# Performance work log

Measured on AMD Instinct MI355X. Metric: run time of the kernel, lower is better.

## Reference

```python
import jax, jax.numpy as jnp
import numpy as np

B, H, W, C = 4, 256, 256, 128
HEADS, WS, SHIFT = 4, 8, 4
EPS = 1e-5


def _rel_pos_index(ws):
    coords = np.stack(np.meshgrid(np.arange(ws), np.arange(ws), indexing='ij'))
    cf = coords.reshape(2, -1)
    rel = (cf[:, :, None] - cf[:, None, :]).transpose(1, 2, 0)
    rel[:, :, 0] += ws - 1
    rel[:, :, 1] += ws - 1
    rel[:, :, 0] *= 2 * ws - 1
    return rel.sum(-1).reshape(-1)

REL_IDX = jnp.array(_rel_pos_index(WS))


def _shift_mask(h, w, ws, shift):
    img = np.zeros((1, h, w, 1))
    cnt = 0
    sl = (slice(0, -ws), slice(-ws, -shift), slice(-shift, None))
    for hs in sl:
        for wsl in sl:
            img[:, hs, wsl, :] = cnt
            cnt += 1
    m = img.reshape(1, h // ws, ws, w // ws, ws, 1).transpose(0, 1, 3, 2, 4, 5).reshape(-1, ws * ws)
    am = m[:, None, :] - m[:, :, None]
    return jnp.array(np.where(am != 0, -100.0, 0.0).astype(np.float32))

ATTN_MASK = _shift_mask(H, W, WS, SHIFT)  # (nW, ws*ws, ws*ws)


def _ln(x, scale, bias):
    mu = x.mean(-1, keepdims=True)
    var = x.var(-1, keepdims=True)
    return (x - mu) / jnp.sqrt(var + EPS) * scale + bias


def setup_inputs() -> dict:
    key = jax.random.key(0)
    ks = jax.random.split(key, 8)
    s = 0.02
    return dict(
        hidden_states=jax.random.normal(ks[0], (B, H * W, C), jnp.float32),
        ln1_scale=jnp.ones((C,), jnp.float32), ln1_bias=jnp.zeros((C,), jnp.float32),
        q_w=jax.random.normal(ks[1], (C, C), jnp.float32) * s, q_b=jnp.zeros((C,), jnp.float32),
        k_w=jax.random.normal(ks[2], (C, C), jnp.float32) * s, k_b=jnp.zeros((C,), jnp.float32),
        v_w=jax.random.normal(ks[3], (C, C), jnp.float32) * s, v_b=jnp.zeros((C,), jnp.float32),
        proj_w=jax.random.normal(ks[4], (C, C), jnp.float32) * s, proj_b=jnp.zeros((C,), jnp.float32),
        rpb_table=jax.random.normal(ks[5], ((2 * WS - 1) ** 2, HEADS), jnp.float32) * s,
        ln2_scale=jnp.ones((C,), jnp.float32), ln2_bias=jnp.zeros((C,), jnp.float32),
        fc1_w=jax.random.normal(ks[6], (C, 4 * C), jnp.float32) * s, fc1_b=jnp.zeros((4 * C,), jnp.float32),
        fc2_w=jax.random.normal(ks[7], (4 * C, C), jnp.float32) * s, fc2_b=jnp.zeros((C,), jnp.float32),
    )


def reference(hidden_states, ln1_scale, ln1_bias, q_w, q_b, k_w, k_b, v_w, v_b,
              proj_w, proj_b, rpb_table, ln2_scale, ln2_bias, fc1_w, fc1_b, fc2_w, fc2_b):
    hd = C // HEADS
    T = WS * WS
    nW = (H // WS) * (W // WS)
    shortcut = hidden_states
    x = _ln(hidden_states, ln1_scale, ln1_bias).reshape(B, H, W, C)
    # cyclic shift
    x = jnp.roll(x, (-SHIFT, -SHIFT), axis=(1, 2))
    # window partition -> (B*nW, T, C)
    x = x.reshape(B, H // WS, WS, W // WS, WS, C).transpose(0, 1, 3, 2, 4, 5).reshape(-1, T, C)
    q = (x @ q_w + q_b).reshape(-1, T, HEADS, hd) / jnp.sqrt(jnp.float32(hd))
    k = (x @ k_w + k_b).reshape(-1, T, HEADS, hd)
    v = (x @ v_w + v_b).reshape(-1, T, HEADS, hd)
    attn = jnp.einsum('bqhd,bkhd->bhqk', q, k)
    bias = rpb_table[REL_IDX].reshape(T, T, HEADS).transpose(2, 0, 1)  # (h, q, k)
    attn = attn + bias[None]
    # shift mask per window
    attn = attn.reshape(B, nW, HEADS, T, T) + ATTN_MASK[None, :, None]
    attn = jax.nn.softmax(attn.reshape(-1, HEADS, T, T), axis=-1)
    out = jnp.einsum('bhqk,bkhd->bqhd', attn, v).reshape(-1, T, C)
    out = out @ proj_w + proj_b
    # window reverse + un-shift
    out = out.reshape(B, H // WS, W // WS, WS, WS, C).transpose(0, 1, 3, 2, 4, 5).reshape(B, H, W, C)
    out = jnp.roll(out, (SHIFT, SHIFT), axis=(1, 2)).reshape(B, H * W, C)
    x = shortcut + out
    y = _ln(x, ln2_scale, ln2_bias)
    y = jax.nn.gelu(y @ fc1_w + fc1_b, approximate=False) @ fc2_w + fc2_b
    return x + y
```

## Files before the change

### kernel.cpp

```cpp
#include <hip/hip_runtime.h>
#include <hip/hip_bf16.h>
#include <math.h>

#define B_ 4
#define H_ 256
#define W_ 256
#define C_ 128
#define HEADS_ 4
#define HD_ 32
#define WS_ 8
#define SHIFT_ 4
#define T_ 64
#define NW_ 1024
#define M_ (B_*NW_*T_)

typedef float floatx4 __attribute__((ext_vector_type(4)));
typedef short bf16x8 __attribute__((ext_vector_type(8)));
typedef unsigned short ushort8v __attribute__((ext_vector_type(8)));
typedef unsigned int uint4v __attribute__((ext_vector_type(4)));

#define MFMA16(a,b,c) __builtin_amdgcn_mfma_f32_16x16x32_bf16(a,b,c,0,0,0)

__device__ __forceinline__ unsigned short f2b(float f){
    union { float f; unsigned int i; } c; c.f = f;
    unsigned int r = c.i + 0x7FFFu + ((c.i >> 16) & 1u);
    return (unsigned short)(r >> 16);
}
__device__ __forceinline__ int region_id(int x){ return (x < 248) ? 0 : ((x < 252) ? 1 : 2); }

__device__ __forceinline__ bf16x8 ldfrag(const unsigned short* p){
    return *(const bf16x8*)p;
}
__device__ __forceinline__ bf16x8 ldfrag_strided(const unsigned short* p, int stride){
    ushort8v u;
    #pragma unroll
    for (int j = 0; j < 8; j++) u[j] = p[j*stride];
    return __builtin_bit_cast(bf16x8, u);
}
__device__ __forceinline__ floatx4 fzero(){ floatx4 v = {0.f,0.f,0.f,0.f}; return v; }

__device__ __forceinline__ float erf_fast(float z){
    float az = fabsf(z);
    float t = 1.0f / fmaf(0.3275911f, az, 1.0f);
    float poly = t*(0.254829592f + t*(-0.284496736f + t*(1.421413741f +
                 t*(-1.453152027f + t*1.061405429f))));
    float e = __expf(-z*z);
    float er = 1.0f - poly*e;
    return (z < 0.f) ? -er : er;
}

#define WSO_QT   0
#define WSO_KT   16384
#define WSO_VT   32768
#define WSO_PT   49152
#define WSO_W1T  65536
#define WSO_W2T  131072
#define WSO_BIAS 196608
#define WS_BYTES_NEEDED (196608u*2u + 16384u*4u)

__global__ __launch_bounds__(256) void prep_weights_kernel(
        const float* __restrict__ qw, const float* __restrict__ kw,
        const float* __restrict__ vw, const float* __restrict__ pw,
        const float* __restrict__ fc1, const float* __restrict__ fc2,
        const float* __restrict__ rpb, unsigned short* __restrict__ ws)
{
    int tid = blockIdx.x * 256 + threadIdx.x;
    int nt = gridDim.x * 256;
    for (int i = tid; i < 16384; i += nt) {
        int n = i >> 7, k = i & 127;
        ws[WSO_QT + i] = f2b(qw[k*128 + n]);
        ws[WSO_KT + i] = f2b(kw[k*128 + n]);
        ws[WSO_VT + i] = f2b(vw[k*128 + n]);
        ws[WSO_PT + i] = f2b(pw[k*128 + n]);
    }
    for (int i = tid; i < 65536; i += nt) {
        int n = i >> 7, k = i & 127;
        ws[WSO_W1T + i] = f2b(fc1[(size_t)k*512 + n]);
    }
    for (int i = tid; i < 65536; i += nt) {
        int n = i >> 9, k = i & 511;
        ws[WSO_W2T + i] = f2b(fc2[(size_t)k*128 + n]);
    }
    float* bt = (float*)(ws + WSO_BIAS);
    for (int i = tid; i < 16384; i += nt) {
        int h = i >> 12, q = (i >> 6) & 63, k = i & 63;
        int th = q >> 3, tw = q & 7, jh = k >> 3, jw = k & 7;
        bt[i] = rpb[((th - jh + 7)*15 + (tw - jw + 7))*HEADS_ + h];
    }
}

__device__ __forceinline__ void gemm64x128_g(
        const unsigned short (*Xs)[136], const unsigned short* __restrict__ Wt,
        int wv, int quad, int l15, floatx4 acc[4][2])
{
    #pragma unroll
    for (int c = 0; c < 4; c++) {
        bf16x8 bf0 = ldfrag(Wt + (size_t)(32*wv + l15)*128      + c*32 + quad*8);
        bf16x8 bf1 = ldfrag(Wt + (size_t)(32*wv + 16 + l15)*128 + c*32 + quad*8);
        #pragma unroll
        for (int m = 0; m < 4; m++) {
            bf16x8 af = ldfrag(&Xs[16*m + l15][c*32 + quad*8]);
            acc[m][0] = MFMA16(af, bf0, acc[m][0]);
            acc[m][1] = MFMA16(af, bf1, acc[m][1]);
        }
    }
}

__global__ __launch_bounds__(256) void swin_attn_kernel3(
        const float* __restrict__ hidden,
        const float* __restrict__ ln1_s, const float* __restrict__ ln1_b,
        const float* __restrict__ q_b, const float* __restrict__ k_b,
        const float* __restrict__ v_b, const float* __restrict__ p_b,
        const unsigned short* __restrict__ wsu,
        float* __restrict__ xres)
{
    __shared__ __align__(16) unsigned short SH[2][T_][136];
    unsigned short (*Xs)[136] = SH[0];
    unsigned short (*Ks)[136] = SH[1];

    int tid = threadIdx.x;
    int wv = tid >> 6, lane = tid & 63;
    int quad = lane >> 4, l15 = lane & 15;
    int gw = blockIdx.x;
    int wi = gw & (NW_-1), b = gw >> 10;
    int hb = wi >> 5, wb = wi & 31;

    {
        int rloc = lane >> 2;
        int t = wv*16 + rloc;
        int th = t >> 3, tw = t & 7;
        int h = (hb*8 + th + SHIFT_) & 255;
        int w = (wb*8 + tw + SHIFT_) & 255;
        int c0 = (lane & 3) * 32;
        const float* xp = hidden + ((size_t)((b<<16) + (h<<8) + w)) * C_ + c0;
        float4 xv[8];
        float s = 0.f, ss = 0.f;
        #pragma unroll
        for (int i = 0; i < 8; i++) {
            xv[i] = *((const float4*)xp + i);
            s  += xv[i].x + xv[i].y + xv[i].z + xv[i].w;
            ss += xv[i].x*xv[i].x + xv[i].y*xv[i].y + xv[i].z*xv[i].z + xv[i].w*xv[i].w;
        }
        s  += __shfl_xor(s, 1, 64);  s  += __shfl_xor(s, 2, 64);
        ss += __shfl_xor(ss, 1, 64); ss += __shfl_xor(ss, 2, 64);
        float mean = s * (1.0f/C_);
        float var  = ss * (1.0f/C_) - mean*mean;
        float rstd = rsqrtf(var + 1e-5f);
        #pragma unroll
        for (int i = 0; i < 8; i++) {
            float4 sc = *((const float4*)(ln1_s + c0) + i);
            float4 bi = *((const float4*)(ln1_b + c0) + i);
            ushort4 o;
            o.x = f2b((xv[i].x - mean)*rstd*sc.x + bi.x);
            o.y = f2b((xv[i].y - mean)*rstd*sc.y + bi.y);
            o.z = f2b((xv[i].z - mean)*rstd*sc.z + bi.z);
            o.w = f2b((xv[i].w - mean)*rstd*sc.w + bi.w);
            *(ushort4*)&Xs[t][c0 + 4*i] = o;
        }
    }
    __syncthreads();

    unsigned int vpk[4][2][2];
    {
        floatx4 kacc[4][2], vacc[4][2];
        #pragma unroll
        for (int m = 0; m < 4; m++) {
            kacc[m][0] = fzero(); kacc[m][1] = fzero();
            vacc[m][0] = fzero(); vacc[m][1] = fzero();
        }
        const unsigned short* Kt = wsu + WSO_KT;
        const unsigned short* Vt = wsu + WSO_VT;
        #pragma unroll
        for (int c = 0; c < 4; c++) {
            size_t off0 = (size_t)(32*wv + l15)*128      + c*32 + quad*8;
            size_t off1 = (size_t)(32*wv + 16 + l15)*128 + c*32 + quad*8;
            bf16x8 kb0 = ldfrag(Kt + off0), kb1 = ldfrag(Kt + off1);
            bf16x8 vb0 = ldfrag(Vt + off0), vb1 = ldfrag(Vt + off1);
            #pragma unroll
            for (int m = 0; m < 4; m++) {
                bf16x8 af = ldfrag(&Xs[16*m + l15][c*32 + quad*8]);
                kacc[m][0] = MFMA16(af, kb0, kacc[m][0]);
                kacc[m][1] = MFMA16(af, kb1, kacc[m][1]);
                vacc[m][0] = MFMA16(af, vb0, vacc[m][0]);
                vacc[m][1] = MFMA16(af, vb1, vacc[m][1]);
            }
        }
        float kb0 = k_b[32*wv + l15], kb1 = k_b[32*wv + 16 + l15];
        float vb0 = v_b[32*wv + l15], vb1 = v_b[32*wv + 16 + l15];
        #pragma unroll
        for (int m = 0; m < 4; m++) {
            #pragma unroll
            for (int r = 0; r < 4; r++) {
                int q = 16*m + 4*quad + r;
                Ks[q][32*wv + l15]      = f2b(kacc[m][0][r] + kb0);
                Ks[q][32*wv + 16 + l15] = f2b(kacc[m][1][r] + kb1);
            }
            vpk[m][0][0] = (unsigned int)f2b(vacc[m][0][0] + vb0)
                         | ((unsigned int)f2b(vacc[m][0][1] + vb0) << 16);
            vpk[m][0][1] = (unsigned int)f2b(vacc[m][0][2] + vb0)
                         | ((unsigned int)f2b(vacc[m][0][3] + vb0) << 16);
            vpk[m][1][0] = (unsigned int)f2b(vacc[m][1][0] + vb1)
                         | ((unsigned int)f2b(vacc[m][1][1] + vb1) << 16);
            vpk[m][1][1] = (unsigned int)f2b(vacc[m][1][2] + vb1)
                         | ((unsigned int)f2b(vacc[m][1][3] + vb1) << 16);
        }
    }
    floatx4 qacc[4][2];
    #pragma unroll
    for (int m = 0; m < 4; m++) { qacc[m][0] = fzero(); qacc[m][1] = fzero(); }
    gemm64x128_g(Xs, wsu + WSO_QT, wv, quad, l15, qacc);
    __syncthreads();
    {
        const float sc = 0.17677669529663687f;
        float qb0 = q_b[32*wv + l15], qb1 = q_b[32*wv + 16 + l15];
        #pragma unroll
        for (int m = 0; m < 4; m++)
            #pragma unroll
            for (int r = 0; r < 4; r++) {
                int q = 16*m + 4*quad + r;
                Xs[q][32*wv + l15]      = f2b((qacc[m][0][r] + qb0) * sc);
                Xs[q][32*wv + 16 + l15] = f2b((qacc[m][1][r] + qb1) * sc);
            }
    }

    floatx4 sacc[4][4];
    #pragma unroll
    for (int m = 0; m < 4; m++)
        #pragma unroll
        for (int n = 0; n < 4; n++) sacc[m][n] = fzero();
    {
        bf16x8 qf[4], kf[4];
        #pragma unroll
        for (int m = 0; m < 4; m++) qf[m] = ldfrag(&Xs[16*m + l15][32*wv + quad*8]);
        #pragma unroll
        for (int n = 0; n < 4; n++) kf[n] = ldfrag(&Ks[16*n + l15][32*wv + quad*8]);
        #pragma unroll
        for (int m = 0; m < 4; m++)
            #pragma unroll
            for (int n = 0; n < 4; n++) sacc[m][n] = MFMA16(kf[n], qf[m], sacc[m][n]);
    }
    __syncthreads();

    {
        const float* bt = (const float*)(wsu + WSO_BIAS) + (wv << 12);
        int cidk[4][4];
        #pragma unroll
        for (int n = 0; n < 4; n++)
            #pragma unroll
            for (int r = 0; r < 4; r++) {
                int kt = 16*n + 4*quad + r;
                cidk[n][r] = region_id(hb*8 + (kt >> 3))*3 + region_id(wb*8 + (kt & 7));
            }
        #pragma unroll
        for (int m = 0; m < 4; m++) {
            int q = 16*m + l15;
            int cidq = region_id(hb*8 + (q >> 3))*3 + region_id(wb*8 + (q & 7));
            float v[4][4];
            float mx = -3.0e38f;
            #pragma unroll
            for (int n = 0; n < 4; n++) {
                float4 bv = *(const float4*)(bt + q*64 + 16*n + 4*quad);
                #pragma unroll
                for (int r = 0; r < 4; r++) {
                    float d = sacc[m][n][r] + bv[r];
                    if (cidq != cidk[n][r]) d -= 100.f;
                    v[n][r] = d;
                    mx = fmaxf(mx, d);
                }
            }
            mx = fmaxf(mx, __shfl_xor(mx, 16, 64));
            mx = fmaxf(mx, __shfl_xor(mx, 32, 64));
            float sum = 0.f;
            #pragma unroll
            for (int n = 0; n < 4; n++)
                #pragma unroll
                for (int r = 0; r < 4; r++) { v[n][r] = __expf(v[n][r] - mx); sum += v[n][r]; }
            sum += __shfl_xor(sum, 16, 64);
            sum += __shfl_xor(sum, 32, 64);
            float inv = 1.0f / sum;
            #pragma unroll
            for (int n = 0; n < 4; n++)
                #pragma unroll
                for (int r = 0; r < 4; r++) sacc[m][n][r] = v[n][r] * inv;
        }
    }

    unsigned short* Ph = (wv < 2) ? (&Ks[0][0] + wv*2560) : (&Xs[0][0] + (wv-2)*2560);
    floatx4 oacc[4][2];
    #pragma unroll
    for (int m = 0; m < 4; m++) { oacc[m][0] = fzero(); oacc[m][1] = fzero(); }
    int laneA = 16*(2*(quad & 1)) + l15;
    bool mhi = (quad >= 2);
    #pragma unroll
    for (int kb = 0; kb < 2; kb++) {
        #pragma unroll
        for (int m = 0; m < 4; m++)
            #pragma unroll
            for (int n2 = 0; n2 < 2; n2++)
                #pragma unroll
                for (int r = 0; r < 4; r++)
                    Ph[(16*m + l15)*40 + n2*16 + 4*quad + r] = f2b(sacc[m][2*kb + n2][r]);
        bf16x8 bfr[2];
        #pragma unroll
        for (int u = 0; u < 2; u++) {
            unsigned int a0m0 = (unsigned int)__shfl((int)vpk[2*kb+0][u][0], laneA, 64);
            unsigned int a1m0 = (unsigned int)__shfl((int)vpk[2*kb+0][u][1], laneA, 64);
            unsigned int b0m0 = (unsigned int)__shfl((int)vpk[2*kb+0][u][0], laneA+16, 64);
            unsigned int b1m0 = (unsigned int)__shfl((int)vpk[2*kb+0][u][1], laneA+16, 64);
            unsigned int a0m1 = (unsigned int)__shfl((int)vpk[2*kb+1][u][0], laneA, 64);
            unsigned int a1m1 = (unsigned int)__shfl((int)vpk[2*kb+1][u][1], laneA, 64);
            unsigned int b0m1 = (unsigned int)__shfl((int)vpk[2*kb+1][u][0], laneA+16, 64);
            unsigned int b1m1 = (unsigned int)__shfl((int)vpk[2*kb+1][u][1], laneA+16, 64);
            uint4v uu;
            uu[0] = mhi ? a0m1 : a0m0;
            uu[1] = mhi ? a1m1 : a1m0;
            uu[2] = mhi ? b0m1 : b0m0;
            uu[3] = mhi ? b1m1 : b1m0;
            bfr[u] = __builtin_bit_cast(bf16x8, uu);
        }
        #pragma unroll
        for (int m = 0; m < 4; m++) {
            bf16x8 af = ldfrag(&Ph[(16*m + l15)*40 + quad*8]);
            oacc[m][0] = MFMA16(af, bfr[0], oacc[m][0]);
            oacc[m][1] = MFMA16(af, bfr[1], oacc[m][1]);
        }
    }
    __syncthreads();
    #pragma unroll
    for (int m = 0; m < 4; m++)
        #pragma unroll
        for (int r = 0; r < 4; r++) {
            int q = 16*m + 4*quad + r;
            Xs[q][32*wv + l15]      = f2b(oacc[m][0][r]);
            Xs[q][32*wv + 16 + l15] = f2b(oacc[m][1][r]);
        }
    __syncthreads();
    floatx4 pacc[4][2];
    #pragma unroll
    for (int m = 0; m < 4; m++) { pacc[m][0] = fzero(); pacc[m][1] = fzero(); }
    gemm64x128_g(Xs, wsu + WSO_PT, wv, quad, l15, pacc);
    __syncthreads();
    {
        float* Fb = (float*)&SH[0][0][0];
        float pb0 = p_b[32*wv + l15], pb1 = p_b[32*wv + 16 + l15];
        #pragma unroll
        for (int m = 0; m < 4; m++)
            #pragma unroll
            for (int r = 0; r < 4; r++) {
                int q = 16*m + 4*quad + r;
                Fb[q*128 + 32*wv + l15]      = pacc[m][0][r] + pb0;
                Fb[q*128 + 32*wv + 16 + l15] = pacc[m][1][r] + pb1;
            }
        __syncthreads();
        int t = tid >> 2;
        int cs = (tid & 3) * 32;
        int th = t >> 3, tw = t & 7;
        int h = (hb*8 + th + SHIFT_) & 255;
        int w = (wb*8 + tw + SHIFT_) & 255;
        size_t dst = ((size_t)((b<<16) + (h<<8) + w)) * C_ + cs;
        const float4* hp = (const float4*)(hidden + dst);
        float4* op = (float4*)(xres + dst);
        const float4* fp = (const float4*)(Fb + t*128 + cs);
        #pragma unroll
        for (int i = 0; i < 8; i++) {
            float4 hv = hp[i];
            float4 fv = fp[i];
            float4 o; o.x = hv.x + fv.x; o.y = hv.y + fv.y;
            o.z = hv.z + fv.z; o.w = hv.w + fv.w;
            op[i] = o;
        }
    }
}

__global__ __launch_bounds__(256) void mlp_ln_kernel3(
        float* __restrict__ xio,
        const float* __restrict__ ln2_s, const float* __restrict__ ln2_b,
        const float* __restrict__ b1, const float* __restrict__ b2,
        const unsigned short* __restrict__ wsu)
{
    __shared__ __align__(16) unsigned short As[T_][136];
    __shared__ __align__(16) unsigned short G[2][T_][72];
    const unsigned short* W1t = wsu + WSO_W1T;
    const unsigned short* W2t = wsu + WSO_W2T;
    int tid = threadIdx.x, wv = tid >> 6, lane = tid & 63;
    int quad = lane >> 4, l15 = lane & 15;
    size_t row0 = (size_t)blockIdx.x * 64;

    {
        int rloc = lane >> 2;
        int t = wv*16 + rloc;
        int c0 = (lane & 3) * 32;
        const float* xp = xio + (row0 + t)*C_ + c0;
        float4 xv[8];
        float s = 0.f, ss = 0.f;
        #pragma unroll
        for (int i = 0; i < 8; i++) {
            xv[i] = *((const float4*)xp + i);
            s  += xv[i].x + xv[i].y + xv[i].z + xv[i].w;
            ss += xv[i].x*xv[i].x + xv[i].y*xv[i].y + xv[i].z*xv[i].z + xv[i].w*xv[i].w;
        }
        s  += __shfl_xor(s, 1, 64);  s  += __shfl_xor(s, 2, 64);
        ss += __shfl_xor(ss, 1, 64); ss += __shfl_xor(ss, 2, 64);
        float mean = s * (1.0f/C_);
        float var  = ss * (1.0f/C_) - mean*mean;
        float rstd = rsqrtf(var + 1e-5f);
        #pragma unroll
        for (int i = 0; i < 8; i++) {
            float4 sc = *((const float4*)(ln2_s + c0) + i);
            float4 bi = *((const float4*)(ln2_b + c0) + i);
            ushort4 o;
            o.x = f2b((xv[i].x - mean)*rstd*sc.x + bi.x);
            o.y = f2b((xv[i].y - mean)*rstd*sc.y + bi.y);
            o.z = f2b((xv[i].z - mean)*rstd*sc.z + bi.z);
            o.w = f2b((xv[i].w - mean)*rstd*sc.w + bi.w);
            *(ushort4*)&As[t][c0 + 4*i] = o;
        }
    }
    __syncthreads();

    floatx4 acc2[4][2];
    #pragma unroll
    for (int m = 0; m < 4; m++) { acc2[m][0] = fzero(); acc2[m][1] = fzero(); }

    for (int ch = 0; ch < 8; ch++) {
        int gb = ch & 1;
        floatx4 a1[4];
        #pragma unroll
        for (int m = 0; m < 4; m++) a1[m] = fzero();
        #pragma unroll
        for (int kc = 0; kc < 4; kc++) {
            bf16x8 bf = ldfrag(W1t + (size_t)(ch*64 + 16*wv + l15)*128 + kc*32 + quad*8);
            #pragma unroll
            for (int m = 0; m < 4; m++) {
                bf16x8 af = ldfrag(&As[16*m + l15][kc*32 + quad*8]);
                a1[m] = MFMA16(af, bf, a1[m]);
            }
        }
        {
            int c_rel = 16*wv + l15;
            float bb = b1[ch*64 + c_rel];
            #pragma unroll
            for (int m = 0; m < 4; m++)
                #pragma unroll
                for (int r = 0; r < 4; r++) {
                    float hh = a1[m][r] + bb;
                    float g = 0.5f * hh * (1.0f + erf_fast(hh * 0.70710678118654752f));
                    G[gb][16*m + 4*quad + r][c_rel] = f2b(g);
                }
        }
        __syncthreads();
        #pragma unroll
        for (int ki = 0; ki < 2; ki++) {
            bf16x8 bf0 = ldfrag(W2t + (size_t)(32*wv + l15)*512      + ch*64 + ki*32 + quad*8);
            bf16x8 bf1 = ldfrag(W2t + (size_t)(32*wv + 16 + l15)*512 + ch*64 + ki*32 + quad*8);
            #pragma unroll
            for (int m = 0; m < 4; m++) {
                bf16x8 af = ldfrag(&G[gb][16*m + l15][ki*32 + quad*8]);
                acc2[m][0] = MFMA16(af, bf0, acc2[m][0]);
                acc2[m][1] = MFMA16(af, bf1, acc2[m][1]);
            }
        }
    }
    {
        float bb0 = b2[32*wv + l15], bb1 = b2[32*wv + 16 + l15];
        #pragma unroll
        for (int m = 0; m < 4; m++)
            #pragma unroll
            for (int r = 0; r < 4; r++) {
                size_t rr = row0 + 16*m + 4*quad + r;
                int c0 = 32*wv + l15;
                xio[rr*C_ + c0]      += acc2[m][0][r] + bb0;
                xio[rr*C_ + c0 + 16] += acc2[m][1][r] + bb1;
            }
    }
}


__device__ __forceinline__ void gemm64x128(
        const unsigned short (*Xs)[136], unsigned short (*Wc)[132],
        const float* __restrict__ Wg, int tid, int wv, int quad, int l15,
        floatx4 acc[4][2])
{
    for (int c = 0; c < 4; c++) {
        __syncthreads();
        #pragma unroll
        for (int it = 0; it < 4; it++) {
            int idx = tid + it*256;
            int kk = idx >> 5;
            int n4 = (idx & 31) * 4;
            float4 v = *(const float4*)(Wg + (size_t)(c*32 + kk)*C_ + n4);
            ushort4 o; o.x=f2b(v.x); o.y=f2b(v.y); o.z=f2b(v.z); o.w=f2b(v.w);
            *(ushort4*)&Wc[kk][n4] = o;
        }
        __syncthreads();
        bf16x8 bf0 = ldfrag_strided(&Wc[quad*8][32*wv + l15],      132);
        bf16x8 bf1 = ldfrag_strided(&Wc[quad*8][32*wv + 16 + l15], 132);
        #pragma unroll
        for (int m = 0; m < 4; m++) {
            bf16x8 af = ldfrag(&Xs[16*m + l15][c*32 + quad*8]);
            acc[m][0] = MFMA16(af, bf0, acc[m][0]);
            acc[m][1] = MFMA16(af, bf1, acc[m][1]);
        }
    }
}

__global__ __launch_bounds__(256) void swin_attn_kernel(
        const float* __restrict__ hidden,
        const float* __restrict__ ln1_s, const float* __restrict__ ln1_b,
        const float* __restrict__ q_w, const float* __restrict__ q_b,
        const float* __restrict__ k_w, const float* __restrict__ k_b,
        const float* __restrict__ v_w, const float* __restrict__ v_b,
        const float* __restrict__ p_w, const float* __restrict__ p_b,
        const float* __restrict__ rpb,
        float* __restrict__ xres)
{
    __shared__ unsigned short Xs[T_][136];
    __shared__ unsigned short Ks[T_][136];
    __shared__ unsigned short Vs[T_][134];
    __shared__ __align__(16) unsigned char U[10240];

    unsigned short (*Wc)[132] = (unsigned short(*)[132])U;
    float* rpbf = (float*)U;

    int tid = threadIdx.x;
    int wv = tid >> 6, lane = tid & 63;
    int quad = lane >> 4, l15 = lane & 15;
    int gw = blockIdx.x;
    int wi = gw & (NW_-1), b = gw >> 10;
    int hb = wi >> 5, wb = wi & 31;

    for (int it = 0; it < 16; it++) {
        int t = wv*16 + it;
        int th = t >> 3, tw = t & 7;
        int h = (hb*8 + th + SHIFT_) & 255;
        int w = (wb*8 + tw + SHIFT_) & 255;
        size_t src = ((size_t)((b<<16) + (h<<8) + w)) * C_;
        float2 u = *(const float2*)(hidden + src + 2*lane);
        float x0 = u.x, x1 = u.y;
        float s = x0 + x1, ss = x0*x0 + x1*x1;
        #pragma unroll
        for (int m = 32; m > 0; m >>= 1) {
            s  += __shfl_xor(s,  m, 64);
            ss += __shfl_xor(ss, m, 64);
        }
        float mean = s * (1.0f/C_);
        float var  = ss * (1.0f/C_) - mean*mean;
        float rstd = rsqrtf(var + 1e-5f);
        int c0 = 2*lane;
        ushort2 o;
        o.x = f2b((x0 - mean) * rstd * ln1_s[c0]   + ln1_b[c0]);
        o.y = f2b((x1 - mean) * rstd * ln1_s[c0+1] + ln1_b[c0+1]);
        *(ushort2*)&Xs[t][c0] = o;
    }

    {
        floatx4 acc[4][2];
        #pragma unroll
        for (int m = 0; m < 4; m++) { acc[m][0] = fzero(); acc[m][1] = fzero(); }
        gemm64x128(Xs, Wc, k_w, tid, wv, quad, l15, acc);
        float kb0 = k_b[32*wv + l15], kb1 = k_b[32*wv + 16 + l15];
        #pragma unroll
        for (int m = 0; m < 4; m++)
            #pragma unroll
            for (int r = 0; r < 4; r++) {
                int q = 16*m + 4*quad + r;
                Ks[q][32*wv + l15]      = f2b(acc[m][0][r] + kb0);
                Ks[q][32*wv + 16 + l15] = f2b(acc[m][1][r] + kb1);
            }
    }
    {
        floatx4 acc[4][2];
        #pragma unroll
        for (int m = 0; m < 4; m++) { acc[m][0] = fzero(); acc[m][1] = fzero(); }
        gemm64x128(Xs, Wc, v_w, tid, wv, quad, l15, acc);
        float vb0 = v_b[32*wv + l15], vb1 = v_b[32*wv + 16 + l15];
        #pragma unroll
        for (int m = 0; m < 4; m++)
            #pragma unroll
            for (int r = 0; r < 4; r++) {
                int q = 16*m + 4*quad + r;
                Vs[q][32*wv + l15]      = f2b(acc[m][0][r] + vb0);
                Vs[q][32*wv + 16 + l15] = f2b(acc[m][1][r] + vb1);
            }
    }
    floatx4 qacc[4][2];
    #pragma unroll
    for (int m = 0; m < 4; m++) { qacc[m][0] = fzero(); qacc[m][1] = fzero(); }
    gemm64x128(Xs, Wc, q_w, tid, wv, quad, l15, qacc);
    __syncthreads();
    for (int i = tid; i < 225*HEADS_; i += 256) rpbf[i] = rpb[i];
    {
        const float sc = 0.17677669529663687f;
        float qb0 = q_b[32*wv + l15], qb1 = q_b[32*wv + 16 + l15];
        #pragma unroll
        for (int m = 0; m < 4; m++)
            #pragma unroll
            for (int r = 0; r < 4; r++) {
                int q = 16*m + 4*quad + r;
                Xs[q][32*wv + l15]      = f2b((qacc[m][0][r] + qb0) * sc);
                Xs[q][32*wv + 16 + l15] = f2b((qacc[m][1][r] + qb1) * sc);
            }
    }
    __syncthreads();

    floatx4 sacc[4][4];
    #pragma unroll
    for (int m = 0; m < 4; m++)
        #pragma unroll
        for (int n = 0; n < 4; n++) sacc[m][n] = fzero();
    {
        bf16x8 qf[4], kf[4];
        #pragma unroll
        for (int m = 0; m < 4; m++) qf[m] = ldfrag(&Xs[16*m + l15][32*wv + quad*8]);
        #pragma unroll
        for (int n = 0; n < 4; n++) kf[n] = ldfrag(&Ks[16*n + l15][32*wv + quad*8]);
        #pragma unroll
        for (int m = 0; m < 4; m++)
            #pragma unroll
            for (int n = 0; n < 4; n++) sacc[m][n] = MFMA16(qf[m], kf[n], sacc[m][n]);
    }
    {
        int jh_[4], jw_[4], cidj_[4];
        #pragma unroll
        for (int n = 0; n < 4; n++) {
            int kt = 16*n + l15;
            jh_[n] = kt >> 3; jw_[n] = kt & 7;
            cidj_[n] = region_id(hb*8 + jh_[n])*3 + region_id(wb*8 + jw_[n]);
        }
        #pragma unroll
        for (int m = 0; m < 4; m++)
            #pragma unroll
            for (int r = 0; r < 4; r++) {
                int q = 16*m + 4*quad + r;
                int th = q >> 3, twq = q & 7;
                int cidi = region_id(hb*8 + th)*3 + region_id(wb*8 + twq);
                float v[4];
                #pragma unroll
                for (int n = 0; n < 4; n++) {
                    float d = sacc[m][n][r];
                    d += rpbf[((th - jh_[n] + 7)*15 + (twq - jw_[n] + 7))*HEADS_ + wv];
                    if (cidi != cidj_[n]) d -= 100.f;
                    v[n] = d;
                }
                float mx = fmaxf(fmaxf(v[0],v[1]), fmaxf(v[2],v[3]));
                #pragma unroll
                for (int off = 1; off < 16; off <<= 1) mx = fmaxf(mx, __shfl_xor(mx, off, 64));
                float sum = 0.f;
                #pragma unroll
                for (int n = 0; n < 4; n++) { v[n] = __expf(v[n] - mx); sum += v[n]; }
                #pragma unroll
                for (int off = 1; off < 16; off <<= 1) sum += __shfl_xor(sum, off, 64);
                float inv = 1.0f / sum;
                #pragma unroll
                for (int n = 0; n < 4; n++) sacc[m][n][r] = v[n] * inv;
            }
    }
    __syncthreads();

    unsigned short* Ph = (wv < 2) ? (&Ks[0][0] + wv*2560)
                                  : ((unsigned short*)U + (wv-2)*2560);
    floatx4 oacc[4][2];
    #pragma unroll
    for (int m = 0; m < 4; m++) { oacc[m][0] = fzero(); oacc[m][1] = fzero(); }
    for (int kb = 0; kb < 2; kb++) {
        #pragma unroll
        for (int m = 0; m < 4; m++)
            #pragma unroll
            for (int r = 0; r < 4; r++) {
                int q = 16*m + 4*quad + r;
                Ph[q*40 + l15]      = f2b(sacc[m][2*kb+0][r]);
                Ph[q*40 + 16 + l15] = f2b(sacc[m][2*kb+1][r]);
            }
        __syncthreads();
        bf16x8 bf0 = ldfrag_strided(&Vs[kb*32 + quad*8][32*wv + l15],      134);
        bf16x8 bf1 = ldfrag_strided(&Vs[kb*32 + quad*8][32*wv + 16 + l15], 134);
        #pragma unroll
        for (int m = 0; m < 4; m++) {
            bf16x8 af = ldfrag(&Ph[(16*m + l15)*40 + quad*8]);
            oacc[m][0] = MFMA16(af, bf0, oacc[m][0]);
            oacc[m][1] = MFMA16(af, bf1, oacc[m][1]);
        }
        __syncthreads();
    }
    #pragma unroll
    for (int m = 0; m < 4; m++)
        #pragma unroll
        for (int r = 0; r < 4; r++) {
            int q = 16*m + 4*quad + r;
            Xs[q][32*wv + l15]      = f2b(oacc[m][0][r]);
            Xs[q][32*wv + 16 + l15] = f2b(oacc[m][1][r]);
        }
    {
        floatx4 acc[4][2];
        #pragma unroll
        for (int m = 0; m < 4; m++) { acc[m][0] = fzero(); acc[m][1] = fzero(); }
        gemm64x128(Xs, Wc, p_w, tid, wv, quad, l15, acc);
        float pb0 = p_b[32*wv + l15], pb1 = p_b[32*wv + 16 + l15];
        #pragma unroll
        for (int m = 0; m < 4; m++)
            #pragma unroll
            for (int r = 0; r < 4; r++) {
                int t = 16*m + 4*quad + r;
                int th = t >> 3, tw = t & 7;
                int h = (hb*8 + th + SHIFT_) & 255;
                int w = (wb*8 + tw + SHIFT_) & 255;
                size_t dst = ((size_t)((b<<16) + (h<<8) + w)) * C_;
                int c0 = 32*wv + l15;
                xres[dst + c0]      = hidden[dst + c0]      + acc[m][0][r] + pb0;
                xres[dst + c0 + 16] = hidden[dst + c0 + 16] + acc[m][1][r] + pb1;
            }
    }
}

__global__ __launch_bounds__(256) void mlp_ln_kernel(
        float* __restrict__ xio,
        const float* __restrict__ ln2_s, const float* __restrict__ ln2_b,
        const float* __restrict__ W1, const float* __restrict__ b1,
        const float* __restrict__ W2, const float* __restrict__ b2)
{
    __shared__ unsigned short As[T_][136];
    __shared__ unsigned short G[T_][72];
    __shared__ unsigned short W1c[C_][68];
    __shared__ unsigned short W2c[T_][132];
    int tid = threadIdx.x, wv = tid >> 6, lane = tid & 63;
    int quad = lane >> 4, l15 = lane & 15;
    size_t row0 = (size_t)blockIdx.x * 64;

    for (int it = 0; it < 16; it++) {
        int t = wv*16 + it;
        const float* xp = xio + (row0 + t)*C_;
        float2 u = *(const float2*)(xp + 2*lane);
        float x0 = u.x, x1 = u.y;
        float s = x0 + x1, ss = x0*x0 + x1*x1;
        #pragma unroll
        for (int m = 32; m > 0; m >>= 1) {
            s  += __shfl_xor(s,  m, 64);
            ss += __shfl_xor(ss, m, 64);
        }
        float mean = s * (1.0f/C_);
        float var  = ss * (1.0f/C_) - mean*mean;
        float rstd = rsqrtf(var + 1e-5f);
        int c0 = 2*lane;
        ushort2 o;
        o.x = f2b((x0 - mean) * rstd * ln2_s[c0]   + ln2_b[c0]);
        o.y = f2b((x1 - mean) * rstd * ln2_s[c0+1] + ln2_b[c0+1]);
        *(ushort2*)&As[t][c0] = o;
    }

    floatx4 acc2[4][2];
    #pragma unroll
    for (int m = 0; m < 4; m++) { acc2[m][0] = fzero(); acc2[m][1] = fzero(); }

    for (int ch = 0; ch < 8; ch++) {
        __syncthreads();
        #pragma unroll
        for (int it = 0; it < 8; it++) {
            int idx = tid + it*256;
            int k = idx >> 4, n4 = (idx & 15) * 4;
            float4 v = *(const float4*)(W1 + (size_t)k*512 + ch*64 + n4);
            ushort4 o; o.x=f2b(v.x); o.y=f2b(v.y); o.z=f2b(v.z); o.w=f2b(v.w);
            *(ushort4*)&W1c[k][n4] = o;
        }
        #pragma unroll
        for (int it = 0; it < 8; it++) {
            int idx = tid + it*256;
            int k = idx >> 5, n4 = (idx & 31) * 4;
            float4 v = *(const float4*)(W2 + (size_t)(ch*64 + k)*C_ + n4);
            ushort4 o; o.x=f2b(v.x); o.y=f2b(v.y); o.z=f2b(v.z); o.w=f2b(v.w);
            *(ushort4*)&W2c[k][n4] = o;
        }
        __syncthreads();
        floatx4 a1[4];
        #pragma unroll
        for (int m = 0; m < 4; m++) a1[m] = fzero();
        #pragma unroll
        for (int kc = 0; kc < 4; kc++) {
            bf16x8 bfrag = ldfrag_strided(&W1c[kc*32 + quad*8][16*wv + l15], 68);
            #pragma unroll
            for (int m = 0; m < 4; m++) {
                bf16x8 af = ldfrag(&As[16*m + l15][kc*32 + quad*8]);
                a1[m] = MFMA16(af, bfrag, a1[m]);
            }
        }
        {
            int c_rel = 16*wv + l15;
            float bb = b1[ch*64 + c_rel];
            #pragma unroll
            for (int m = 0; m < 4; m++)
                #pragma unroll
                for (int r = 0; r < 4; r++) {
                    int q = 16*m + 4*quad + r;
                    float hh = a1[m][r] + bb;
                    float g = 0.5f * hh * (1.0f + erff(hh * 0.70710678118654752f));
                    G[q][c_rel] = f2b(g);
                }
        }
        __syncthreads();
        #pragma unroll
        for (int ki = 0; ki < 2; ki++) {
            bf16x8 bf0 = ldfrag_strided(&W2c[ki*32 + quad*8][32*wv + l15],      132);
            bf16x8 bf1 = ldfrag_strided(&W2c[ki*32 + quad*8][32*wv + 16 + l15], 132);
            #pragma unroll
            for (int m = 0; m < 4; m++) {
                bf16x8 af = ldfrag(&G[16*m + l15][ki*32 + quad*8]);
                acc2[m][0] = MFMA16(af, bf0, acc2[m][0]);
                acc2[m][1] = MFMA16(af, bf1, acc2[m][1]);
            }
        }
    }
    {
        float bb0 = b2[32*wv + l15], bb1 = b2[32*wv + 16 + l15];
        #pragma unroll
        for (int m = 0; m < 4; m++)
            #pragma unroll
            for (int r = 0; r < 4; r++) {
                size_t rr = row0 + 16*m + 4*quad + r;
                int c0 = 32*wv + l15;
                xio[rr*C_ + c0]      += acc2[m][0][r] + bb0;
                xio[rr*C_ + c0 + 16] += acc2[m][1][r] + bb1;
            }
    }
}

extern "C" void kernel_launch(void* const* d_in, const int* in_sizes, int n_in,
                              void* d_out, int out_size, void* d_ws, size_t ws_size,
                              hipStream_t stream) {
    (void)in_sizes; (void)n_in; (void)out_size;
    const float* hidden = (const float*)d_in[0];
    const float* ln1_s  = (const float*)d_in[1];
    const float* ln1_b  = (const float*)d_in[2];
    const float* q_w    = (const float*)d_in[3];
    const float* q_b    = (const float*)d_in[4];
    const float* k_w    = (const float*)d_in[5];
    const float* k_b    = (const float*)d_in[6];
    const float* v_w    = (const float*)d_in[7];
    const float* v_b    = (const float*)d_in[8];
    const float* p_w    = (const float*)d_in[9];
    const float* p_b    = (const float*)d_in[10];
    const float* rpb    = (const float*)d_in[11];
    const float* ln2_s  = (const float*)d_in[12];
    const float* ln2_b  = (const float*)d_in[13];
    const float* fc1_w  = (const float*)d_in[14];
    const float* fc1_b  = (const float*)d_in[15];
    const float* fc2_w  = (const float*)d_in[16];
    const float* fc2_b  = (const float*)d_in[17];
    float* outp = (float*)d_out;

    if (d_ws != nullptr && ws_size >= (size_t)WS_BYTES_NEEDED) {
        unsigned short* wsu = (unsigned short*)d_ws;
        prep_weights_kernel<<<64, 256, 0, stream>>>(q_w, k_w, v_w, p_w,
                fc1_w, fc2_w, rpb, wsu);
        swin_attn_kernel3<<<B_*NW_, 256, 0, stream>>>(hidden, ln1_s, ln1_b,
                q_b, k_b, v_b, p_b, wsu, outp);
        mlp_ln_kernel3<<<M_/64, 256, 0, stream>>>(outp, ln2_s, ln2_b,
                fc1_b, fc2_b, wsu);
    } else {
        swin_attn_kernel<<<B_*NW_, 256, 0, stream>>>(hidden, ln1_s, ln1_b,
                q_w, q_b, k_w, k_b, v_w, v_b, p_w, p_b, rpb, outp);
        mlp_ln_kernel<<<M_/64, 256, 0, stream>>>(outp, ln2_s, ln2_b,
                fc1_w, fc1_b, fc2_w, fc2_b);
    }
}
```

Baseline: 619.3 us.

## Stage V and P in dedicated LDS, fuse QKV GEMM, single-buffer GELU tile

The attention kernel now computes Q, K and V in one fused MFMA loop. It stores V in a new shared-memory tile and reads it back with strided loads, replacing the register-packed V and its cross-lane shuffles. Softmax probabilities go to a dedicated per-wave LDS buffer instead of reusing the X/K tiles, which removes two block-wide barriers. The MLP kernel drops the double-buffered GELU tile for a single buffer with an extra barrier, adds a minimum-occupancy launch bound, and swaps in hardware rcp/rsq approximations. These changes trade more LDS in the attention kernel for fewer syncs and shuffles, and trade an extra sync in the MLP kernel for less LDS and higher occupancy.

```diff
diff --git a/kernel.cpp b/kernel.cpp
--- a/kernel.cpp
+++ b/kernel.cpp
@@ -17,7 +17,6 @@
 typedef float floatx4 __attribute__((ext_vector_type(4)));
 typedef short bf16x8 __attribute__((ext_vector_type(8)));
 typedef unsigned short ushort8v __attribute__((ext_vector_type(8)));
-typedef unsigned int uint4v __attribute__((ext_vector_type(4)));
 
 #define MFMA16(a,b,c) __builtin_amdgcn_mfma_f32_16x16x32_bf16(a,b,c,0,0,0)
 
@@ -39,14 +38,16 @@
 }
 __device__ __forceinline__ floatx4 fzero(){ floatx4 v = {0.f,0.f,0.f,0.f}; return v; }
 
-__device__ __forceinline__ float erf_fast(float z){
+__device__ __forceinline__ float gelu_fast(float x){
+    float z = x * 0.70710678118654752f;
     float az = fabsf(z);
-    float t = 1.0f / fmaf(0.3275911f, az, 1.0f);
+    float t = __builtin_amdgcn_rcpf(fmaf(0.3275911f, az, 1.0f));
     float poly = t*(0.254829592f + t*(-0.284496736f + t*(1.421413741f +
                  t*(-1.453152027f + t*1.061405429f))));
     float e = __expf(-z*z);
     float er = 1.0f - poly*e;
-    return (z < 0.f) ? -er : er;
+    er = (z < 0.f) ? -er : er;
+    return 0.5f * x * (1.0f + er);
 }
 
 #define WSO_QT   0
@@ -106,7 +107,7 @@
     }
 }
 
-__global__ __launch_bounds__(256) void swin_attn_kernel3(
+__global__ __launch_bounds__(256) void swin_attn_kernel4(
         const float* __restrict__ hidden,
         const float* __restrict__ ln1_s, const float* __restrict__ ln1_b,
         const float* __restrict__ q_b, const float* __restrict__ k_b,
@@ -115,6 +116,8 @@
         float* __restrict__ xres)
 {
     __shared__ __align__(16) unsigned short SH[2][T_][136];
+    __shared__ __align__(16) unsigned short Vs[T_][134];
+    __shared__ __align__(16) unsigned short PhD[4][2560];
     unsigned short (*Xs)[136] = SH[0];
     unsigned short (*Ks)[136] = SH[1];
 
@@ -145,7 +148,7 @@
         ss += __shfl_xor(ss, 1, 64); ss += __shfl_xor(ss, 2, 64);
         float mean = s * (1.0f/C_);
         float var  = ss * (1.0f/C_) - mean*mean;
-        float rstd = rsqrtf(var + 1e-5f);
+        float rstd = __builtin_amdgcn_rsqf(var + 1e-5f);
         #pragma unroll
         for (int i = 0; i < 8; i++) {
             float4 sc = *((const float4*)(ln1_s + c0) + i);
@@ -160,55 +163,49 @@
     }
     __syncthreads();
 
-    unsigned int vpk[4][2][2];
+    floatx4 qacc[4][2];
     {
         floatx4 kacc[4][2], vacc[4][2];
         #pragma unroll
         for (int m = 0; m < 4; m++) {
+            qacc[m][0] = fzero(); qacc[m][1] = fzero();
             kacc[m][0] = fzero(); kacc[m][1] = fzero();
             vacc[m][0] = fzero(); vacc[m][1] = fzero();
         }
+        const unsigned short* Qt = wsu + WSO_QT;
         const unsigned short* Kt = wsu + WSO_KT;
         const unsigned short* Vt = wsu + WSO_VT;
         #pragma unroll
         for (int c = 0; c < 4; c++) {
             size_t off0 = (size_t)(32*wv + l15)*128      + c*32 + quad*8;
             size_t off1 = (size_t)(32*wv + 16 + l15)*128 + c*32 + quad*8;
-            bf16x8 kb0 = ldfrag(Kt + off0), kb1 = ldfrag(Kt + off1);
-            bf16x8 vb0 = ldfrag(Vt + off0), vb1 = ldfrag(Vt + off1);
+            bf16x8 qf0 = ldfrag(Qt + off0), qf1 = ldfrag(Qt + off1);
+            bf16x8 kf0 = ldfrag(Kt + off0), kf1 = ldfrag(Kt + off1);
+            bf16x8 vf0 = ldfrag(Vt + off0), vf1 = ldfrag(Vt + off1);
             #pragma unroll
             for (int m = 0; m < 4; m++) {
                 bf16x8 af = ldfrag(&Xs[16*m + l15][c*32 + quad*8]);
-                kacc[m][0] = MFMA16(af, kb0, kacc[m][0]);
-                kacc[m][1] = MFMA16(af, kb1, kacc[m][1]);
-                vacc[m][0] = MFMA16(af, vb0, vacc[m][0]);
-                vacc[m][1] = MFMA16(af, vb1, vacc[m][1]);
+                qacc[m][0] = MFMA16(af, qf0, qacc[m][0]);
+                qacc[m][1] = MFMA16(af, qf1, qacc[m][1]);
+                kacc[m][0] = MFMA16(af, kf0, kacc[m][0]);
+                kacc[m][1] = MFMA16(af, kf1, kacc[m][1]);
+                vacc[m][0] = MFMA16(af, vf0, vacc[m][0]);
+                vacc[m][1] = MFMA16(af, vf1, vacc[m][1]);
             }
         }
         float kb0 = k_b[32*wv + l15], kb1 = k_b[32*wv + 16 + l15];
         float vb0 = v_b[32*wv + l15], vb1 = v_b[32*wv + 16 + l15];
         #pragma unroll
-        for (int m = 0; m < 4; m++) {
+        for (int m = 0; m < 4; m++)
             #pragma unroll
             for (int r = 0; r < 4; r++) {
                 int q = 16*m + 4*quad + r;
                 Ks[q][32*wv + l15]      = f2b(kacc[m][0][r] + kb0);
                 Ks[q][32*wv + 16 + l15] = f2b(kacc[m][1][r] + kb1);
-            }
-            vpk[m][0][0] = (unsigned int)f2b(vacc[m][0][0] + vb0)
-                         | ((unsigned int)f2b(vacc[m][0][1] + vb0) << 16);
-            vpk[m][0][1] = (unsigned int)f2b(vacc[m][0][2] + vb0)
-                         | ((unsigned int)f2b(vacc[m][0][3] + vb0) << 16);
-            vpk[m][1][0] = (unsigned int)f2b(vacc[m][1][0] + vb1)
-                         | ((unsigned int)f2b(vacc[m][1][1] + vb1) << 16);
-            vpk[m][1][1] = (unsigned int)f2b(vacc[m][1][2] + vb1)
-                         | ((unsigned int)f2b(vacc[m][1][3] + vb1) << 16);
-        }
-    }
-    floatx4 qacc[4][2];
-    #pragma unroll
-    for (int m = 0; m < 4; m++) { qacc[m][0] = fzero(); qacc[m][1] = fzero(); }
-    gemm64x128_g(Xs, wsu + WSO_QT, wv, quad, l15, qacc);
+                Vs[q][32*wv + l15]      = f2b(vacc[m][0][r] + vb0);
+                Vs[q][32*wv + 16 + l15] = f2b(vacc[m][1][r] + vb1);
+            }
+    }
     __syncthreads();
     {
         const float sc = 0.17677669529663687f;
@@ -239,7 +236,6 @@
             #pragma unroll
             for (int n = 0; n < 4; n++) sacc[m][n] = MFMA16(kf[n], qf[m], sacc[m][n]);
     }
-    __syncthreads();
 
     {
         const float* bt = (const float*)(wsu + WSO_BIAS) + (wv << 12);
@@ -277,7 +273,7 @@
                 for (int r = 0; r < 4; r++) { v[n][r] = __expf(v[n][r] - mx); sum += v[n][r]; }
             sum += __shfl_xor(sum, 16, 64);
             sum += __shfl_xor(sum, 32, 64);
-            float inv = 1.0f / sum;
+            float inv = __builtin_amdgcn_rcpf(sum);
             #pragma unroll
             for (int n = 0; n < 4; n++)
                 #pragma unroll
@@ -285,12 +281,10 @@
         }
     }
 
-    unsigned short* Ph = (wv < 2) ? (&Ks[0][0] + wv*2560) : (&Xs[0][0] + (wv-2)*2560);
+    unsigned short* Ph = PhD[wv];
     floatx4 oacc[4][2];
     #pragma unroll
     for (int m = 0; m < 4; m++) { oacc[m][0] = fzero(); oacc[m][1] = fzero(); }
-    int laneA = 16*(2*(quad & 1)) + l15;
-    bool mhi = (quad >= 2);
     #pragma unroll
     for (int kb = 0; kb < 2; kb++) {
         #pragma unroll
@@ -300,32 +294,15 @@
                 #pragma unroll
                 for (int r = 0; r < 4; r++)
                     Ph[(16*m + l15)*40 + n2*16 + 4*quad + r] = f2b(sacc[m][2*kb + n2][r]);
-        bf16x8 bfr[2];
-        #pragma unroll
-        for (int u = 0; u < 2; u++) {
-            unsigned int a0m0 = (unsigned int)__shfl((int)vpk[2*kb+0][u][0], laneA, 64);
-            unsigned int a1m0 = (unsigned int)__shfl((int)vpk[2*kb+0][u][1], laneA, 64);
-            unsigned int b0m0 = (unsigned int)__shfl((int)vpk[2*kb+0][u][0], laneA+16, 64);
-            unsigned int b1m0 = (unsigned int)__shfl((int)vpk[2*kb+0][u][1], laneA+16, 64);
-            unsigned int a0m1 = (unsigned int)__shfl((int)vpk[2*kb+1][u][0], laneA, 64);
-            unsigned int a1m1 = (unsigned int)__shfl((int)vpk[2*kb+1][u][1], laneA, 64);
-            unsigned int b0m1 = (unsigned int)__shfl((int)vpk[2*kb+1][u][0], laneA+16, 64);
-            unsigned int b1m1 = (unsigned int)__shfl((int)vpk[2*kb+1][u][1], laneA+16, 64);
-            uint4v uu;
-            uu[0] = mhi ? a0m1 : a0m0;
-            uu[1] = mhi ? a1m1 : a1m0;
-            uu[2] = mhi ? b0m1 : b0m0;
-            uu[3] = mhi ? b1m1 : b1m0;
-            bfr[u] = __builtin_bit_cast(bf16x8, uu);
-        }
+        bf16x8 bf0 = ldfrag_strided(&Vs[kb*32 + quad*8][32*wv + l15],      134);
+        bf16x8 bf1 = ldfrag_strided(&Vs[kb*32 + quad*8][32*wv + 16 + l15], 134);
         #pragma unroll
         for (int m = 0; m < 4; m++) {
             bf16x8 af = ldfrag(&Ph[(16*m + l15)*40 + quad*8]);
-            oacc[m][0] = MFMA16(af, bfr[0], oacc[m][0]);
-            oacc[m][1] = MFMA16(af, bfr[1], oacc[m][1]);
-        }
-    }
-    __syncthreads();
+            oacc[m][0] = MFMA16(af, bf0, oacc[m][0]);
+            oacc[m][1] = MFMA16(af, bf1, oacc[m][1]);
+        }
+    }
     #pragma unroll
     for (int m = 0; m < 4; m++)
         #pragma unroll
@@ -372,14 +349,14 @@
     }
 }
 
-__global__ __launch_bounds__(256) void mlp_ln_kernel3(
+__global__ __launch_bounds__(256, 6) void mlp_ln_kernel4(
         float* __restrict__ xio,
         const float* __restrict__ ln2_s, const float* __restrict__ ln2_b,
         const float* __restrict__ b1, const float* __restrict__ b2,
         const unsigned short* __restrict__ wsu)
 {
     __shared__ __align__(16) unsigned short As[T_][136];
-    __shared__ __align__(16) unsigned short G[2][T_][72];
+    __shared__ __align__(16) unsigned short G[T_][72];
     const unsigned short* W1t = wsu + WSO_W1T;
     const unsigned short* W2t = wsu + WSO_W2T;
     int tid = threadIdx.x, wv = tid >> 6, lane = tid & 63;
@@ -403,7 +380,7 @@
         ss += __shfl_xor(ss, 1, 64); ss += __shfl_xor(ss, 2, 64);
         float mean = s * (1.0f/C_);
         float var  = ss * (1.0f/C_) - mean*mean;
-        float rstd = rsqrtf(var + 1e-5f);
+        float rstd = __builtin_amdgcn_rsqf(var + 1e-5f);
         #pragma unroll
         for (int i = 0; i < 8; i++) {
             float4 sc = *((const float4*)(ln2_s + c0) + i);
@@ -423,7 +400,6 @@
     for (int m = 0; m < 4; m++) { acc2[m][0] = fzero(); acc2[m][1] = fzero(); }
 
     for (int ch = 0; ch < 8; ch++) {
-        int gb = ch & 1;
         floatx4 a1[4];
         #pragma unroll
         for (int m = 0; m < 4; m++) a1[m] = fzero();
@@ -436,6 +412,7 @@
                 a1[m] = MFMA16(af, bf, a1[m]);
             }
         }
+        __syncthreads();
         {
             int c_rel = 16*wv + l15;
             float bb = b1[ch*64 + c_rel];
@@ -444,8 +421,7 @@
                 #pragma unroll
                 for (int r = 0; r < 4; r++) {
                     float hh = a1[m][r] + bb;
-                    float g = 0.5f * hh * (1.0f + erf_fast(hh * 0.70710678118654752f));
-                    G[gb][16*m + 4*quad + r][c_rel] = f2b(g);
+                    G[16*m + 4*quad + r][c_rel] = f2b(gelu_fast(hh));
                 }
         }
         __syncthreads();
@@ -455,7 +431,7 @@
             bf16x8 bf1 = ldfrag(W2t + (size_t)(32*wv + 16 + l15)*512 + ch*64 + ki*32 + quad*8);
             #pragma unroll
             for (int m = 0; m < 4; m++) {
-                bf16x8 af = ldfrag(&G[gb][16*m + l15][ki*32 + quad*8]);
+                bf16x8 af = ldfrag(&G[16*m + l15][ki*32 + quad*8]);
                 acc2[m][0] = MFMA16(af, bf0, acc2[m][0]);
                 acc2[m][1] = MFMA16(af, bf1, acc2[m][1]);
             }
@@ -850,9 +826,9 @@
         unsigned short* wsu = (unsigned short*)d_ws;
         prep_weights_kernel<<<64, 256, 0, stream>>>(q_w, k_w, v_w, p_w,
                 fc1_w, fc2_w, rpb, wsu);
-        swin_attn_kernel3<<<B_*NW_, 256, 0, stream>>>(hidden, ln1_s, ln1_b,
+        swin_attn_kernel4<<<B_*NW_, 256, 0, stream>>>(hidden, ln1_s, ln1_b,
                 q_b, k_b, v_b, p_b, wsu, outp);
-        mlp_ln_kernel3<<<M_/64, 256, 0, stream>>>(outp, ln2_s, ln2_b,
+        mlp_ln_kernel4<<<M_/64, 256, 0, stream>>>(outp, ln2_s, ln2_b,
                 fc1_b, fc2_b, wsu);
     } else {
         swin_attn_kernel<<<B_*NW_, 256, 0, stream>>>(hidden, ln1_s, ln1_b,
```

Result: faster. 577.1 us (-6.8%).
